# Kernel optimization log

Measured on AMD Instinct MI355X. Metric: run time of the kernel, lower is better.

The kernel has to match this reference:

```python
import jax, jax.numpy as jnp
import numpy as np


def setup_inputs() -> dict:
    key = jax.random.key(0)
    k1, k2, k3 = jax.random.split(key, 3)
    N, K = 131072, 1000
    f = jax.random.normal(k1, (N, K), dtype=jnp.float32)
    ccp = jax.random.uniform(k2, (K,), dtype=jnp.float32)
    labels = jax.random.randint(k3, (N,), 0, K, dtype=jnp.int32)
    return {"f": f, "ccp": ccp, "labels": labels, "K": K}


def reference(f, ccp, labels, K):
    # neglog[i, j] = -log_softmax(f)[i, j]
    neglog = -jax.nn.log_softmax(f, axis=1)  # [N, K]
    N = f.shape[0]
    # Per-class counts and per-class column sums (segmented reduction by label).
    counts = jax.ops.segment_sum(jnp.ones((N,), dtype=f.dtype), labels, num_segments=K)  # [K]
    sums = jax.ops.segment_sum(neglog, labels, num_segments=K)  # [K, K]
    # means[k] = mean over rows with label==k; classes with zero samples contribute 0
    # (the torch loop skips them entirely).
    safe_counts = jnp.maximum(counts, 1.0)
    means = jnp.where(counts[:, None] > 0, sums / safe_counts[:, None], 0.0)  # [K, K]
    # loss_vector = sum_k ccp[k] * means[k] ; temp[k] = -(K-1)*ccp[k]*means[k,k]
    loss_vector = ccp @ means - (K - 1) * ccp * jnp.diagonal(means)  # [K]
    # beta = +inf => max(loss_vector, -inf) == loss_vector
    final_loss = jnp.sum(loss_vector)
    weighted = counts * loss_vector  # count * loss_vector as in torch code
    return final_loss, weighted
```

## Files before the change

### kernel.cpp

```cpp
#include <hip/hip_runtime.h>
#include <math.h>


typedef float f4 __attribute__((ext_vector_type(4)));

__device__ inline float wave_reduce_sum(float v) {
    #pragma unroll
    for (int off = 32; off > 0; off >>= 1)
        v += __shfl_xor(v, off, 64);
    return v;
}

__global__ __launch_bounds__(256) void count_kernel(const int* __restrict__ labels,
                                                    float* __restrict__ counts,
                                                    int N, int K) {
    __shared__ int h[1024];
    for (int j = threadIdx.x; j < 1024; j += blockDim.x) h[j] = 0;
    __syncthreads();
    for (int i = blockIdx.x * blockDim.x + threadIdx.x; i < N;
         i += gridDim.x * blockDim.x) {
        atomicAdd(&h[labels[i]], 1);
    }
    __syncthreads();
    for (int j = threadIdx.x; j < K; j += blockDim.x) {
        int c = h[j];
        if (c) atomicAdd(&counts[j], (float)c);
    }
}

template <int V4>
__global__ __launch_bounds__(256) void main_kernel(
    const float* __restrict__ f, const int* __restrict__ labels,
    const float* __restrict__ ccp, const float* __restrict__ counts,
    float* __restrict__ g_multi, float* __restrict__ d_multi,
    float* __restrict__ S_acc, int N, int K) {
    __shared__ float g_sh[1024];
    __shared__ float d_sh[1024];
    __shared__ float s_sh[4];

    const int tid = threadIdx.x;
    const int lane = tid & 63;
    const int wid = tid >> 6;
    const int gwid = blockIdx.x * 4 + wid;
    const int nwaves = gridDim.x * 4;
    const int K4 = K >> 2;

    for (int j = tid; j < 1024; j += 256) { g_sh[j] = 0.f; d_sh[j] = 0.f; }
    __syncthreads();

    f4 gacc[V4];
    #pragma unroll
    for (int t = 0; t < V4; ++t) gacc[t] = (f4)(0.f);
    float s_reg = 0.f;

    f4 valsA[V4], valsB[V4], valsC[V4];
    float wA = 0.f, wB = 0.f, wC = 0.f;
    int lA = 0, lB = 0, lC = 0;

    auto issue = [&](f4 (&vals)[V4], float& w, int& l, int r) {
        const f4* row4 = reinterpret_cast<const f4*>(f + (size_t)r * (size_t)K);
        #pragma unroll
        for (int t = 0; t < V4; ++t) {
            int j4 = lane + 64 * t;
            vals[t] = (j4 < K4) ? __builtin_nontemporal_load(&row4[j4]) : (f4)(0.f);
        }
        l = labels[r];
        w = ccp[l] / counts[l];
    };

    auto process = [&](f4 (&vals)[V4], float w, int l) {
        float e = 0.f;
        #pragma unroll
        for (int t = 0; t < V4; ++t) {
            int j4 = lane + 64 * t;
            if (j4 < K4) {
                e += __expf(vals[t].x) + __expf(vals[t].y) +
                     __expf(vals[t].z) + __expf(vals[t].w);
                gacc[t].x = fmaf(w, vals[t].x, gacc[t].x);
                gacc[t].y = fmaf(w, vals[t].y, gacc[t].y);
                gacc[t].z = fmaf(w, vals[t].z, gacc[t].z);
                gacc[t].w = fmaf(w, vals[t].w, gacc[t].w);
            }
        }
        e = wave_reduce_sum(e);
        float lse = __logf(e);
        const int j4l = l >> 2;
        const int ll = j4l & 63;
        const int tl = j4l >> 6;
        const int cl = l & 3;
        #pragma unroll
        for (int t = 0; t < V4; ++t) {
            if (lane == ll && t == tl) {
                float vl = (cl == 0) ? vals[t].x
                         : (cl == 1) ? vals[t].y
                         : (cl == 2) ? vals[t].z : vals[t].w;
                atomicAdd(&d_sh[l], lse - vl);
            }
        }
        if (lane == 0) s_reg = fmaf(w, lse, s_reg);
    };

    int rA = gwid;
    int rB = rA + nwaves;
    int rC = rB + nwaves;
    if (rA < N) {
        issue(valsA, wA, lA, rA);
        if (rB < N) issue(valsB, wB, lB, rB);
        while (true) {
            if (rC < N) issue(valsC, wC, lC, rC);
            process(valsA, wA, lA);
            rA = rC + nwaves;
            if (rB >= N) break;
            if (rA < N) issue(valsA, wA, lA, rA);
            process(valsB, wB, lB);
            rB = rA + nwaves;
            if (rC >= N) break;
            if (rB < N) issue(valsB, wB, lB, rB);
            process(valsC, wC, lC);
            rC = rB + nwaves;
            if (rA >= N) break;
        }
    }

    if (lane == 0) s_sh[wid] = s_reg;
    #pragma unroll
    for (int t = 0; t < V4; ++t) {
        int j4 = lane + 64 * t;
        if (j4 < K4) {
            atomicAdd(&g_sh[4 * j4 + 0], gacc[t].x);
            atomicAdd(&g_sh[4 * j4 + 1], gacc[t].y);
            atomicAdd(&g_sh[4 * j4 + 2], gacc[t].z);
            atomicAdd(&g_sh[4 * j4 + 3], gacc[t].w);
        }
    }
    __syncthreads();
    const int part = (blockIdx.x & 7) * 1024;
    for (int j = tid; j < K; j += 256) {
        atomicAdd(&g_multi[part + j], g_sh[j]);
        atomicAdd(&d_multi[part + j], d_sh[j]);
    }
    if (tid == 0) {
        atomicAdd(S_acc, s_sh[0] + s_sh[1] + s_sh[2] + s_sh[3]);
    }
}

__global__ __launch_bounds__(1024) void finalize_kernel(
    const float* __restrict__ ccp, const float* __restrict__ counts,
    const float* __restrict__ g_multi, const float* __restrict__ d_multi,
    const float* __restrict__ S_acc, float* __restrict__ out, int K) {
    __shared__ float red[16];
    const int j = threadIdx.x;
    const float S = S_acc[0];

    float lv = 0.f;
    if (j < K) {
        float gj = 0.f, dj = 0.f;
        #pragma unroll
        for (int c = 0; c < 8; ++c) {
            gj += g_multi[c * 1024 + j];
            dj += d_multi[c * 1024 + j];
        }
        float cnt = counts[j];
        float dm = (cnt > 0.f) ? dj / cnt : 0.f;
        float val = S - gj - (float)(K - 1) * ccp[j] * dm;
        lv = val;
        out[1 + j] = cnt * val;
    }

    float v = wave_reduce_sum(lv);
    const int lane = j & 63;
    const int wv = j >> 6;
    if (lane == 0) red[wv] = v;
    __syncthreads();
    if (j == 0) {
        float tot = 0.f;
        for (int w2 = 0; w2 < 16; ++w2) tot += red[w2];
        out[0] = tot;
    }
}

extern "C" void kernel_launch(void* const* d_in, const int* in_sizes, int n_in,
                              void* d_out, int out_size, void* d_ws, size_t ws_size,
                              hipStream_t stream) {
    const float* f = (const float*)d_in[0];
    const float* ccp = (const float*)d_in[1];
    const int* labels = (const int*)d_in[2];
    const int K = in_sizes[1];
    const int N = in_sizes[2];

    float* ws = (float*)d_ws;
    float* counts = ws;
    float* g_multi = ws + 1024;
    float* d_multi = ws + 1024 + 8192;
    float* S_acc = ws + 1024 + 16384;
    float* out = (float*)d_out;

    (void)hipMemsetAsync(d_ws, 0, (size_t)(1024 + 16384 + 1) * sizeof(float), stream);

    count_kernel<<<256, 256, 0, stream>>>(labels, counts, N, K);
    main_kernel<4><<<1024, 256, 0, stream>>>(f, labels, ccp, counts, g_multi,
                                             d_multi, S_acc, N, K);
    finalize_kernel<<<1, 1024, 0, stream>>>(ccp, counts, g_multi, d_multi, S_acc,
                                            out, K);
}
```

Measured before the change: 125.6 us.

## Fuse finalize into main kernel via last-block counter; scalarize per-row weight

The separate finalize kernel is removed. The last block to finish the main kernel, detected with an atomic done counter and thread fences, now computes the per-class outputs and the total. The per-row weight lookup moves from the load stage to the process stage and uses a readfirstlane'd label, so it becomes a scalar load and fewer registers are held live across the pipeline. The exp reduction is also split from the FMA accumulation loop. This saves one kernel launch and its gap, at the cost of fence and atomic overhead in every block and a serialized tail on a single block.

```diff
diff --git a/kernel.cpp b/kernel.cpp
--- a/kernel.cpp
+++ b/kernel.cpp
@@ -33,10 +33,13 @@
     const float* __restrict__ f, const int* __restrict__ labels,
     const float* __restrict__ ccp, const float* __restrict__ counts,
     float* __restrict__ g_multi, float* __restrict__ d_multi,
-    float* __restrict__ S_acc, int N, int K) {
+    float* __restrict__ S_acc, int* __restrict__ done_ctr,
+    float* __restrict__ out, int N, int K) {
     __shared__ float g_sh[1024];
     __shared__ float d_sh[1024];
     __shared__ float s_sh[4];
+    __shared__ float red[4];
+    __shared__ int is_last;
 
     const int tid = threadIdx.x;
     const int lane = tid & 63;
@@ -54,10 +57,9 @@
     float s_reg = 0.f;
 
     f4 valsA[V4], valsB[V4], valsC[V4];
-    float wA = 0.f, wB = 0.f, wC = 0.f;
     int lA = 0, lB = 0, lC = 0;
 
-    auto issue = [&](f4 (&vals)[V4], float& w, int& l, int r) {
+    auto issue = [&](f4 (&vals)[V4], int& l, int r) {
         const f4* row4 = reinterpret_cast<const f4*>(f + (size_t)r * (size_t)K);
         #pragma unroll
         for (int t = 0; t < V4; ++t) {
@@ -65,10 +67,11 @@
             vals[t] = (j4 < K4) ? __builtin_nontemporal_load(&row4[j4]) : (f4)(0.f);
         }
         l = labels[r];
-        w = ccp[l] / counts[l];
     };
 
-    auto process = [&](f4 (&vals)[V4], float w, int l) {
+    auto process = [&](f4 (&vals)[V4], int l) {
+        const int ls = __builtin_amdgcn_readfirstlane(l);
+        const float w = ccp[ls] / counts[ls];
         float e = 0.f;
         #pragma unroll
         for (int t = 0; t < V4; ++t) {
@@ -76,25 +79,31 @@
             if (j4 < K4) {
                 e += __expf(vals[t].x) + __expf(vals[t].y) +
                      __expf(vals[t].z) + __expf(vals[t].w);
+            }
+        }
+        e = wave_reduce_sum(e);
+        float lse = __logf(e);
+        #pragma unroll
+        for (int t = 0; t < V4; ++t) {
+            int j4 = lane + 64 * t;
+            if (j4 < K4) {
                 gacc[t].x = fmaf(w, vals[t].x, gacc[t].x);
                 gacc[t].y = fmaf(w, vals[t].y, gacc[t].y);
                 gacc[t].z = fmaf(w, vals[t].z, gacc[t].z);
                 gacc[t].w = fmaf(w, vals[t].w, gacc[t].w);
             }
         }
-        e = wave_reduce_sum(e);
-        float lse = __logf(e);
-        const int j4l = l >> 2;
+        const int j4l = ls >> 2;
         const int ll = j4l & 63;
         const int tl = j4l >> 6;
-        const int cl = l & 3;
+        const int cl = ls & 3;
         #pragma unroll
         for (int t = 0; t < V4; ++t) {
             if (lane == ll && t == tl) {
                 float vl = (cl == 0) ? vals[t].x
                          : (cl == 1) ? vals[t].y
                          : (cl == 2) ? vals[t].z : vals[t].w;
-                atomicAdd(&d_sh[l], lse - vl);
+                atomicAdd(&d_sh[ls], lse - vl);
             }
         }
         if (lane == 0) s_reg = fmaf(w, lse, s_reg);
@@ -104,19 +113,19 @@
     int rB = rA + nwaves;
     int rC = rB + nwaves;
     if (rA < N) {
-        issue(valsA, wA, lA, rA);
-        if (rB < N) issue(valsB, wB, lB, rB);
+        issue(valsA, lA, rA);
+        if (rB < N) issue(valsB, lB, rB);
         while (true) {
-            if (rC < N) issue(valsC, wC, lC, rC);
-            process(valsA, wA, lA);
+            if (rC < N) issue(valsC, lC, rC);
+            process(valsA, lA);
             rA = rC + nwaves;
             if (rB >= N) break;
-            if (rA < N) issue(valsA, wA, lA, rA);
-            process(valsB, wB, lB);
+            if (rA < N) issue(valsA, lA, rA);
+            process(valsB, lB);
             rB = rA + nwaves;
             if (rC >= N) break;
-            if (rB < N) issue(valsB, wB, lB, rB);
-            process(valsC, wC, lC);
+            if (rB < N) issue(valsB, lB, rB);
+            process(valsC, lC);
             rC = rB + nwaves;
             if (rA >= N) break;
         }
@@ -142,40 +151,38 @@
     if (tid == 0) {
         atomicAdd(S_acc, s_sh[0] + s_sh[1] + s_sh[2] + s_sh[3]);
     }
-}
-
-__global__ __launch_bounds__(1024) void finalize_kernel(
-    const float* __restrict__ ccp, const float* __restrict__ counts,
-    const float* __restrict__ g_multi, const float* __restrict__ d_multi,
-    const float* __restrict__ S_acc, float* __restrict__ out, int K) {
-    __shared__ float red[16];
-    const int j = threadIdx.x;
-    const float S = S_acc[0];
-
-    float lv = 0.f;
-    if (j < K) {
-        float gj = 0.f, dj = 0.f;
-        #pragma unroll
-        for (int c = 0; c < 8; ++c) {
-            gj += g_multi[c * 1024 + j];
-            dj += d_multi[c * 1024 + j];
-        }
-        float cnt = counts[j];
-        float dm = (cnt > 0.f) ? dj / cnt : 0.f;
-        float val = S - gj - (float)(K - 1) * ccp[j] * dm;
-        lv = val;
-        out[1 + j] = cnt * val;
-    }
-
-    float v = wave_reduce_sum(lv);
-    const int lane = j & 63;
-    const int wv = j >> 6;
-    if (lane == 0) red[wv] = v;
-    __syncthreads();
-    if (j == 0) {
-        float tot = 0.f;
-        for (int w2 = 0; w2 < 16; ++w2) tot += red[w2];
-        out[0] = tot;
+
+    __threadfence();
+    if (tid == 0) {
+        int done = atomicAdd(done_ctr, 1);
+        is_last = (done == (int)gridDim.x - 1);
+    }
+    __syncthreads();
+    if (is_last) {
+        __threadfence();
+        const float S = S_acc[0];
+        float lvsum = 0.f;
+        #pragma unroll
+        for (int q = 0; q < 4; ++q) {
+            int j = tid + q * 256;
+            if (j < K) {
+                float gj = 0.f, dj = 0.f;
+                #pragma unroll
+                for (int c = 0; c < 8; ++c) {
+                    gj += g_multi[c * 1024 + j];
+                    dj += d_multi[c * 1024 + j];
+                }
+                float cnt = counts[j];
+                float dm = (cnt > 0.f) ? dj / cnt : 0.f;
+                float val = S - gj - (float)(K - 1) * ccp[j] * dm;
+                lvsum += val;
+                out[1 + j] = cnt * val;
+            }
+        }
+        float v = wave_reduce_sum(lvsum);
+        if (lane == 0) red[wid] = v;
+        __syncthreads();
+        if (tid == 0) out[0] = red[0] + red[1] + red[2] + red[3];
     }
 }
 
@@ -191,15 +198,14 @@
     float* ws = (float*)d_ws;
     float* counts = ws;
     float* g_multi = ws + 1024;
-    float* d_multi = ws + 1024 + 8192;
-    float* S_acc = ws + 1024 + 16384;
+    float* d_multi = ws + 9216;
+    float* S_acc = ws + 17408;
+    int* done_ctr = (int*)(ws + 17409);
     float* out = (float*)d_out;
 
-    (void)hipMemsetAsync(d_ws, 0, (size_t)(1024 + 16384 + 1) * sizeof(float), stream);
+    (void)hipMemsetAsync(d_ws, 0, (size_t)17410 * sizeof(float), stream);
 
     count_kernel<<<256, 256, 0, stream>>>(labels, counts, N, K);
     main_kernel<4><<<1024, 256, 0, stream>>>(f, labels, ccp, counts, g_multi,
-                                             d_multi, S_acc, N, K);
-    finalize_kernel<<<1, 1024, 0, stream>>>(ccp, counts, g_multi, d_multi, S_acc,
-                                            out, K);
-}
+                                             d_multi, S_acc, done_ctr, out, N, K);
+}
```

After: 302.8 us. 2.41x slower.
